# Kernel tuning notes

Measured on AMD Instinct MI355X. Metric: run time of the kernel, lower is better.

## Reference

```python
import jax, jax.numpy as jnp
import numpy as np

N_FEATURE = 1024
N_HEAD = 16
DK = N_FEATURE // N_HEAD
SCALE = float(np.sqrt(DK))
LN_EPS = 1e-5


def setup_inputs() -> dict:
    key = jax.random.key(0)
    ks = jax.random.split(key, 12)
    B, T, F = 4, 2048, N_FEATURE
    s = 1.0 / np.sqrt(F)
    inp = {
        "key": jax.random.normal(ks[0], (B, T, F), jnp.float32),
        "value": jax.random.normal(ks[1], (B, T, F), jnp.float32),
        "query": jax.random.normal(ks[2], (B, T, F), jnp.float32),
        "Wq": jax.random.uniform(ks[3], (F, F), jnp.float32, -s, s),
        "bq": jax.random.uniform(ks[4], (F,), jnp.float32, -s, s),
        "Wk": jax.random.uniform(ks[5], (F, F), jnp.float32, -s, s),
        "bk": jax.random.uniform(ks[6], (F,), jnp.float32, -s, s),
        "Wv": jax.random.uniform(ks[7], (F, F), jnp.float32, -s, s),
        "bv": jax.random.uniform(ks[8], (F,), jnp.float32, -s, s),
        "Wo": jax.random.uniform(ks[9], (F, F), jnp.float32, -s, s),
        "bo": jax.random.uniform(ks[10], (F,), jnp.float32, -s, s),
        "ln_g": jnp.ones((F,), jnp.float32),
        "ln_b": jnp.zeros((F,), jnp.float32),
    }
    return inp


def reference(key, value, query, Wq, bq, Wk, bk, Wv, bv, Wo, bo, ln_g, ln_b):
    # key/value/query: [B, T, F]. torch chunk(n_head, -1) == reshape to (B,T,H,dk).
    B, T, F = query.shape
    residual = query
    q = (query @ Wq.T + bq).reshape(B, T, N_HEAD, DK)
    k = (key @ Wk.T + bk).reshape(B, T, N_HEAD, DK)
    v = (value @ Wv.T + bv).reshape(B, T, N_HEAD, DK)
    # scores: [B, H, Tq, Tk]
    scores = jnp.einsum("bqhd,bkhd->bhqk", q, k) / SCALE
    attn = jax.nn.softmax(scores, axis=-1)
    ctx = jnp.einsum("bhqk,bkhd->bqhd", attn, v).reshape(B, T, F)
    out = ctx @ Wo.T + bo  # dropout in eval mode = identity
    x = residual + out
    mu = jnp.mean(x, axis=-1, keepdims=True)
    var = jnp.mean(jnp.square(x - mu), axis=-1, keepdims=True)
    return (x - mu) * jax.lax.rsqrt(var + LN_EPS) * ln_g + ln_b
```

## Files before the change

kernel.cpp:

```cpp
#include <hip/hip_runtime.h>
#include <hip/hip_bf16.h>
#include <cstdint>
#include <cstddef>

#define DEVI __device__ __forceinline__

typedef __attribute__((ext_vector_type(8))) short short8;
typedef __attribute__((ext_vector_type(4))) float f32x4;
typedef __attribute__((ext_vector_type(16))) float f32x16;
typedef __attribute__((ext_vector_type(4))) unsigned int u32x4;

constexpr int Bz = 4, Tt = 2048, Fd = 1024, Hh = 16, Dk = 64;
constexpr int Mrows = Bz * Tt;
constexpr float QSCALE = 0.18033688011112042f;

DEVI unsigned short f2bf(float f) {
  union { __hip_bfloat16 h; unsigned short u; } cv;
  cv.h = __float2bfloat16(f);
  return cv.u;
}

DEVI unsigned cvtpk(float a, float b) {
  unsigned r;
  asm("v_cvt_pk_bf16_f32 %0, %1, %2" : "=v"(r) : "v"(a), "v"(b));
  return r;
}

DEVI void gl_lds16(const void* g, void* s) {
  __builtin_amdgcn_global_load_lds(
      (const __attribute__((address_space(1))) void*)g,
      (__attribute__((address_space(3))) void*)s, 16, 0, 0);
}

__global__ void cvt4_bf16(const float* __restrict__ s0, unsigned short* __restrict__ d0,
                          const float* __restrict__ s1, unsigned short* __restrict__ d1,
                          const float* __restrict__ s2, unsigned short* __restrict__ d2,
                          const float* __restrict__ s3, unsigned short* __restrict__ d3,
                          int n4) {
  const float* src = blockIdx.y == 0 ? s0 : (blockIdx.y == 1 ? s1 : (blockIdx.y == 2 ? s2 : s3));
  unsigned short* dst = blockIdx.y == 0 ? d0 : (blockIdx.y == 1 ? d1 : (blockIdx.y == 2 ? d2 : d3));
  int i = blockIdx.x * blockDim.x + threadIdx.x;
  int stride = gridDim.x * blockDim.x;
  for (; i < n4; i += stride) {
    float4 v = reinterpret_cast<const float4*>(src)[i];
    ushort4 o;
    o.x = f2bf(v.x); o.y = f2bf(v.y); o.z = f2bf(v.z); o.w = f2bf(v.w);
    reinterpret_cast<ushort4*>(dst)[i] = o;
  }
}

__global__ __launch_bounds__(256, 2) void gemm_qkvf(
    const float* __restrict__ q32, const float* __restrict__ k32,
    const float* __restrict__ v32, const unsigned short* __restrict__ wq,
    const unsigned short* __restrict__ wk, const unsigned short* __restrict__ wv,
    const float* __restrict__ bq, const float* __restrict__ bk, const float* __restrict__ bv,
    unsigned short* __restrict__ Qb, unsigned short* __restrict__ Kb,
    unsigned short* __restrict__ Vt) {
  constexpr int K = 1024, N = 1024;
  __shared__ __align__(16) unsigned short As[128 * 64];
  __shared__ __align__(16) unsigned short Bs[128 * 64];
  int z = blockIdx.z;
  const float* A32 = z == 0 ? q32 : (z == 1 ? k32 : v32);
  const unsigned short* W = z == 0 ? wq : (z == 1 ? wk : wv);
  const float* bias = z == 0 ? bq : (z == 1 ? bk : bv);
  void* out = z == 0 ? (void*)Qb : (z == 1 ? (void*)Kb : (void*)Vt);
  float scale = z == 0 ? QSCALE : 1.0f;
  int mode = z == 2 ? 2 : 0;

  int f = blockIdx.y * gridDim.x + blockIdx.x;
  f = (f & 7) * 64 + (f >> 3);
  const int m0 = (f >> 3) * 128, n0 = (f & 7) * 128;
  const int t = threadIdx.x, w = t >> 6, l = t & 63;
  const int wr = w >> 1, wc = w & 1;
  const int lr = l & 15, lg = l >> 4;
  f32x4 acc[4][4] = {};

  for (int k0 = 0; k0 < K; k0 += 64) {
    __syncthreads();
    float4 fA[4][2];
#pragma unroll
    for (int i = 0; i < 4; ++i) {
      int row = i * 32 + w * 8 + (l >> 3);
      const float* src = A32 + (size_t)(m0 + row) * K + k0 + (l & 7) * 8;
      fA[i][0] = ((const float4*)src)[0];
      fA[i][1] = ((const float4*)src)[1];
    }
#pragma unroll
    for (int i = 0; i < 4; ++i) {
      int base = i * 4096 + w * 1024;
      int d = base + l * 16;
      int row = d >> 7;
      int srcb = ((l & 7) ^ (row & 7)) << 4;
      gl_lds16((const char*)W + ((size_t)(n0 + row) * K + k0) * 2 + srcb, (char*)Bs + base);
    }
#pragma unroll
    for (int i = 0; i < 4; ++i) {
      int row = i * 32 + w * 8 + (l >> 3);
      u32x4 wv4;
      wv4[0] = cvtpk(fA[i][0].x, fA[i][0].y);
      wv4[1] = cvtpk(fA[i][0].z, fA[i][0].w);
      wv4[2] = cvtpk(fA[i][1].x, fA[i][1].y);
      wv4[3] = cvtpk(fA[i][1].z, fA[i][1].w);
      int slot = (l & 7) ^ (row & 7);
      *(u32x4*)((char*)As + row * 128 + slot * 16) = wv4;
    }
    __syncthreads();
#pragma unroll
    for (int kk = 0; kk < 2; ++kk) {
      short8 af[4], bf[4];
#pragma unroll
      for (int i = 0; i < 4; ++i) {
        int ra = wr * 64 + i * 16 + lr;
        int rb = wc * 64 + i * 16 + lr;
        af[i] = *(const short8*)((const char*)As + ra * 128 + (((kk * 4 + lg) ^ (ra & 7)) << 4));
        bf[i] = *(const short8*)((const char*)Bs + rb * 128 + (((kk * 4 + lg) ^ (rb & 7)) << 4));
      }
#pragma unroll
      for (int mi = 0; mi < 4; ++mi)
#pragma unroll
        for (int ni = 0; ni < 4; ++ni)
          acc[mi][ni] = __builtin_amdgcn_mfma_f32_16x16x32_bf16(af[mi], bf[ni], acc[mi][ni], 0, 0, 0);
    }
  }
#pragma unroll
  for (int mi = 0; mi < 4; ++mi)
#pragma unroll
    for (int ni = 0; ni < 4; ++ni) {
      int col = n0 + wc * 64 + ni * 16 + lr;
      float bv = bias[col];
      if (mode == 2) {
        int hh = col >> 6, dd = col & 63;
        int row = m0 + wr * 64 + mi * 16 + lg * 4;
        int bb = row >> 11, t0 = row & 2047;
        ushort4 o;
        o.x = f2bf(acc[mi][ni][0] + bv);
        o.y = f2bf(acc[mi][ni][1] + bv);
        o.z = f2bf(acc[mi][ni][2] + bv);
        o.w = f2bf(acc[mi][ni][3] + bv);
        *(ushort4*)((unsigned short*)out + (((size_t)(bb * Hh + hh) * Dk + dd) << 11) + t0) = o;
      } else {
#pragma unroll
        for (int r = 0; r < 4; ++r) {
          int row = m0 + wr * 64 + mi * 16 + lg * 4 + r;
          ((unsigned short*)out)[(size_t)row * N + col] = f2bf((acc[mi][ni][r] + bv) * scale);
        }
      }
    }
}

__global__ __launch_bounds__(256, 2) void gemm_out(
    const unsigned short* __restrict__ A, const unsigned short* __restrict__ W,
    const float* __restrict__ bias, const float* __restrict__ resid,
    float* __restrict__ out) {
  constexpr int K = 1024, N = 1024;
  __shared__ __align__(16) unsigned short As[128 * 64];
  __shared__ __align__(16) unsigned short Bs[128 * 64];
  int f = blockIdx.y * gridDim.x + blockIdx.x;
  f = (f & 7) * 64 + (f >> 3);
  const int m0 = (f >> 3) * 128, n0 = (f & 7) * 128;
  const int t = threadIdx.x, w = t >> 6, l = t & 63;
  const int wr = w >> 1, wc = w & 1;
  const int lr = l & 15, lg = l >> 4;
  f32x4 acc[4][4] = {};
  for (int k0 = 0; k0 < K; k0 += 64) {
    __syncthreads();
#pragma unroll
    for (int i = 0; i < 4; ++i) {
      int base = i * 4096 + w * 1024;
      int d = base + l * 16;
      int row = d >> 7;
      int srcb = ((l & 7) ^ (row & 7)) << 4;
      gl_lds16((const char*)A + ((size_t)(m0 + row) * K + k0) * 2 + srcb, (char*)As + base);
      gl_lds16((const char*)W + ((size_t)(n0 + row) * K + k0) * 2 + srcb, (char*)Bs + base);
    }
    __syncthreads();
#pragma unroll
    for (int kk = 0; kk < 2; ++kk) {
      short8 af[4], bf[4];
#pragma unroll
      for (int i = 0; i < 4; ++i) {
        int ra = wr * 64 + i * 16 + lr;
        int rb = wc * 64 + i * 16 + lr;
        af[i] = *(const short8*)((const char*)As + ra * 128 + (((kk * 4 + lg) ^ (ra & 7)) << 4));
        bf[i] = *(const short8*)((const char*)Bs + rb * 128 + (((kk * 4 + lg) ^ (rb & 7)) << 4));
      }
#pragma unroll
      for (int mi = 0; mi < 4; ++mi)
#pragma unroll
        for (int ni = 0; ni < 4; ++ni)
          acc[mi][ni] = __builtin_amdgcn_mfma_f32_16x16x32_bf16(af[mi], bf[ni], acc[mi][ni], 0, 0, 0);
    }
  }
#pragma unroll
  for (int mi = 0; mi < 4; ++mi)
#pragma unroll
    for (int ni = 0; ni < 4; ++ni) {
      int col = n0 + wc * 64 + ni * 16 + lr;
      float bv = bias[col];
#pragma unroll
      for (int r = 0; r < 4; ++r) {
        int row = m0 + wr * 64 + mi * 16 + lg * 4 + r;
        size_t idx = (size_t)row * N + col;
        out[idx] = acc[mi][ni][r] + bv + resid[idx];
      }
    }
}

__global__ __launch_bounds__(256, 2) void attn_kernel(
    const unsigned short* __restrict__ Qb, const unsigned short* __restrict__ Kb,
    const unsigned short* __restrict__ Vt, unsigned short* __restrict__ Ctx) {
  __shared__ __align__(16) unsigned short smem[6 * 4096];
  unsigned short* Ks0 = smem;
  unsigned short* Ks1 = smem + 4096;
  unsigned short* Ks2 = smem + 2 * 4096;
  unsigned short* Vs0 = smem + 3 * 4096;
  unsigned short* Vs1 = smem + 4 * 4096;
  unsigned short* Vs2 = smem + 5 * 4096;
  int bid = blockIdx.x;
  bid = (bid & 7) * 64 + (bid >> 3);
  const int q0 = (bid & 7) * 256;
  const int h = (bid >> 3) & 15;
  const int b = bid >> 7;
  const int t = threadIdx.x, w = t >> 6, l = t & 63;
  const int q31 = l & 31, hi = l >> 5;
  const int qbase = q0 + w * 64;

  short8 qfA[4], qfB[4];
  {
    const unsigned short* qpA = Qb + (size_t)(b * Tt + qbase + q31) * Fd + h * Dk;
    const unsigned short* qpB = qpA + (size_t)32 * Fd;
#pragma unroll
    for (int c = 0; c < 4; ++c) {
      qfA[c] = *(const short8*)(qpA + c * 16 + hi * 8);
      qfB[c] = *(const short8*)(qpB + c * 16 + hi * 8);
    }
  }

  int koff[8];
#pragma unroll
  for (int g = 0; g < 2; ++g)
#pragma unroll
    for (int c = 0; c < 4; ++c) {
      int row = g * 32 + q31;
      koff[g * 4 + c] = row * 128 + ((c * 32 + hi * 16) ^ ((row & 7) << 4));
    }

  const size_t kbase = (size_t)(b * Tt) * Fd + h * Dk;
  const size_t vbase = (size_t)((b * Hh + h) * Dk) * Tt;

  f32x16 OA0{}, OA1{}, OB0{}, OB1{};
  float lsA0 = 0.f, lsB0 = 0.f, lsA1 = 0.f, lsB1 = 0.f;

  auto stage = [&](unsigned short* Kd, unsigned short* Vd, int kt) {
#pragma unroll
    for (int i = 0; i < 2; ++i) {
      int base = w * 2048 + i * 1024;
      int d0 = base + l * 16;
      int row = d0 >> 7, inb = d0 & 127;
      int srcb = inb ^ ((row & 7) << 4);
      gl_lds16((const char*)Kb + (kbase + (size_t)(kt * 64 + row) * Fd) * 2 + srcb, (char*)Kd + base);
      gl_lds16((const char*)Vt + (vbase + (size_t)row * Tt + kt * 64) * 2 + srcb, (char*)Vd + base);
    }
  };

  auto softmax_pack = [&](const f32x16& S0, const f32x16& S1, float& lsA, float& lsB, short8* pf) {
    unsigned pk0[8], pk1[8];
#pragma unroll
    for (int j = 0; j < 8; ++j) {
      int r = j * 2;
      float a0 = __builtin_amdgcn_exp2f(S0[r]);
      float a1 = __builtin_amdgcn_exp2f(S0[r + 1]);
      float b0 = __builtin_amdgcn_exp2f(S1[r]);
      float b1 = __builtin_amdgcn_exp2f(S1[r + 1]);
      lsA += a0 + a1;
      lsB += b0 + b1;
      pk0[j] = cvtpk(a0, a1);
      pk1[j] = cvtpk(b0, b1);
    }
#pragma unroll
    for (int kc = 0; kc < 2; ++kc) {
      unsigned a0 = pk0[kc * 4 + 0], a2 = pk0[kc * 4 + 2];
      unsigned a1 = pk0[kc * 4 + 1], a3 = pk0[kc * 4 + 3];
      asm("v_permlane32_swap_b32 %0, %1" : "+v"(a0), "+v"(a2));
      asm("v_permlane32_swap_b32 %0, %1" : "+v"(a1), "+v"(a3));
      unsigned b0 = pk1[kc * 4 + 0], b2 = pk1[kc * 4 + 2];
      unsigned b1 = pk1[kc * 4 + 1], b3 = pk1[kc * 4 + 3];
      asm("v_permlane32_swap_b32 %0, %1" : "+v"(b0), "+v"(b2));
      asm("v_permlane32_swap_b32 %0, %1" : "+v"(b1), "+v"(b3));
      u32x4 fa, fb;
      fa[0] = a0; fa[1] = a1; fa[2] = a2; fa[3] = a3;
      fb[0] = b0; fb[1] = b1; fb[2] = b2; fb[3] = b3;
      pf[kc] = __builtin_bit_cast(short8, fa);
      pf[2 + kc] = __builtin_bit_cast(short8, fb);
    }
  };

  auto tile = [&](const unsigned short* Kd, const unsigned short* Vd) {
    f32x16 S0a{}, S1a{}, S0b{}, S1b{};
    __builtin_amdgcn_s_setprio(1);
#pragma unroll
    for (int c = 0; c < 4; ++c) {
      short8 k0 = *(const short8*)((const char*)Kd + koff[c]);
      short8 k1 = *(const short8*)((const char*)Kd + koff[4 + c]);
      S0a = __builtin_amdgcn_mfma_f32_32x32x16_bf16(k0, qfA[c], S0a, 0, 0, 0);
      S1a = __builtin_amdgcn_mfma_f32_32x32x16_bf16(k1, qfA[c], S1a, 0, 0, 0);
      S0b = __builtin_amdgcn_mfma_f32_32x32x16_bf16(k0, qfB[c], S0b, 0, 0, 0);
      S1b = __builtin_amdgcn_mfma_f32_32x32x16_bf16(k1, qfB[c], S1b, 0, 0, 0);
    }
    __builtin_amdgcn_s_setprio(0);
    short8 pfA[4], pfB[4];
    softmax_pack(S0a, S1a, lsA0, lsB0, pfA);
    softmax_pack(S0b, S1b, lsA1, lsB1, pfB);
    __builtin_amdgcn_s_setprio(1);
#pragma unroll
    for (int db = 0; db < 2; ++db)
#pragma unroll
      for (int kvc = 0; kvc < 4; ++kvc) {
        short8 vf = *(const short8*)((const char*)Vd + koff[db * 4 + kvc]);
        if (db == 0) {
          OA0 = __builtin_amdgcn_mfma_f32_32x32x16_bf16(vf, pfA[kvc], OA0, 0, 0, 0);
          OB0 = __builtin_amdgcn_mfma_f32_32x32x16_bf16(vf, pfB[kvc], OB0, 0, 0, 0);
        } else {
          OA1 = __builtin_amdgcn_mfma_f32_32x32x16_bf16(vf, pfA[kvc], OA1, 0, 0, 0);
          OB1 = __builtin_amdgcn_mfma_f32_32x32x16_bf16(vf, pfB[kvc], OB1, 0, 0, 0);
        }
      }
    __builtin_amdgcn_s_setprio(0);
  };

  stage(Ks0, Vs0, 0);
  stage(Ks1, Vs1, 1);
  unsigned short *kC = Ks0, *vC = Vs0;
  unsigned short *kN = Ks1, *vN = Vs1;
  unsigned short *kW = Ks2, *vW = Vs2;
  for (int kt = 0; kt < 30; ++kt) {
    asm volatile("s_waitcnt vmcnt(4)" ::: "memory");
    __builtin_amdgcn_s_barrier();
    stage(kW, vW, kt + 2);
    tile(kC, vC);
    unsigned short *tk = kC, *tv = vC;
    kC = kN; vC = vN;
    kN = kW; vN = vW;
    kW = tk; vW = tv;
  }
  asm volatile("s_waitcnt vmcnt(4)" ::: "memory");
  __builtin_amdgcn_s_barrier();
  tile(kC, vC);
  asm volatile("s_waitcnt vmcnt(0)" ::: "memory");
  __builtin_amdgcn_s_barrier();
  tile(kN, vN);
  __builtin_amdgcn_s_barrier();

  float ls0 = lsA0 + lsB0;
  ls0 += __shfl_xor(ls0, 32);
  float linv0 = 1.0f / ls0;
  float ls1 = lsA1 + lsB1;
  ls1 += __shfl_xor(ls1, 32);
  float linv1 = 1.0f / ls1;
  unsigned short* Ow = smem + w * 4096;
#pragma unroll
  for (int g = 0; g < 2; ++g) {
    float linv = g == 0 ? linv0 : linv1;
    int rowq = g * 32 + q31;
#pragma unroll
    for (int db = 0; db < 2; ++db)
#pragma unroll
      for (int rp = 0; rp < 8; ++rp) {
        int r = rp * 2;
        float a, b2;
        if (g == 0) {
          a = (db == 0 ? OA0[r] : OA1[r]) * linv;
          b2 = (db == 0 ? OA0[r + 1] : OA1[r + 1]) * linv;
        } else {
          a = (db == 0 ? OB0[r] : OB1[r]) * linv;
          b2 = (db == 0 ? OB0[r + 1] : OB1[r + 1]) * linv;
        }
        unsigned wv = cvtpk(a, b2);
        int dd = db * 32 + (r & 3) + 8 * (r >> 2) + 4 * hi;
        int byteo = (rowq * 128 + (dd >> 1) * 4) ^ ((rowq & 7) << 4);
        *(unsigned*)((char*)Ow + byteo) = wv;
      }
  }
#pragma unroll
  for (int i = 0; i < 8; ++i) {
    int qq = i * 8 + (l >> 3), slot = l & 7;
    int byteo = (qq * 128 + slot * 16) ^ ((qq & 7) << 4);
    short8 ov = *(const short8*)((const char*)Ow + byteo);
    *(short8*)(Ctx + (size_t)(b * Tt + qbase + qq) * Fd + h * Dk + slot * 8) = ov;
  }
}

__global__ __launch_bounds__(256) void ln_res(
    float* __restrict__ xo, const float* __restrict__ gamma, const float* __restrict__ beta) {
  int row = blockIdx.x, t = threadIdx.x;
  float4 xv = ((const float4*)(xo + (size_t)row * Fd))[t];
  float x0 = xv.x, x1 = xv.y, x2 = xv.z, x3 = xv.w;
  float s = x0 + x1 + x2 + x3;
  float ss = x0 * x0 + x1 * x1 + x2 * x2 + x3 * x3;
#pragma unroll
  for (int off = 32; off >= 1; off >>= 1) {
    s += __shfl_xor(s, off);
    ss += __shfl_xor(ss, off);
  }
  __shared__ float rs_[4], rss[4];
  int w = t >> 6, l = t & 63;
  if (l == 0) { rs_[w] = s; rss[w] = ss; }
  __syncthreads();
  s = rs_[0] + rs_[1] + rs_[2] + rs_[3];
  ss = rss[0] + rss[1] + rss[2] + rss[3];
  float mu = s * (1.0f / 1024.0f);
  float var = ss * (1.0f / 1024.0f) - mu * mu;
  float rstd = rsqrtf(var + 1e-5f);
  float4 gv = ((const float4*)gamma)[t];
  float4 bv = ((const float4*)beta)[t];
  float4 o;
  o.x = (x0 - mu) * rstd * gv.x + bv.x;
  o.y = (x1 - mu) * rstd * gv.y + bv.y;
  o.z = (x2 - mu) * rstd * gv.z + bv.z;
  o.w = (x3 - mu) * rstd * gv.w + bv.w;
  ((float4*)(xo + (size_t)row * Fd))[t] = o;
}

extern "C" void kernel_launch(void* const* d_in, const int* in_sizes, int n_in,
                              void* d_out, int out_size, void* d_ws, size_t ws_size,
                              hipStream_t stream) {
  (void)in_sizes; (void)n_in; (void)out_size; (void)ws_size;
  const float* key   = (const float*)d_in[0];
  const float* value = (const float*)d_in[1];
  const float* query = (const float*)d_in[2];
  const float* Wq = (const float*)d_in[3];
  const float* bq = (const float*)d_in[4];
  const float* Wk = (const float*)d_in[5];
  const float* bk = (const float*)d_in[6];
  const float* Wv = (const float*)d_in[7];
  const float* bv_ = (const float*)d_in[8];
  const float* Wo = (const float*)d_in[9];
  const float* bo = (const float*)d_in[10];
  const float* ln_g = (const float*)d_in[11];
  const float* ln_b = (const float*)d_in[12];
  float* out = (float*)d_out;

  char* ws = (char*)d_ws;
  size_t off = 0;
  auto alloc = [&](size_t bytes) {
    char* p = ws + off;
    off += (bytes + 255) & ~(size_t)255;
    return p;
  };
  const size_t MF = (size_t)Mrows * Fd;
  unsigned short* Qb  = (unsigned short*)alloc(MF * 2);
  unsigned short* Kbf = (unsigned short*)alloc(MF * 2);
  unsigned short* Vtb = (unsigned short*)alloc(MF * 2);
  unsigned short* Ctx = (unsigned short*)alloc(MF * 2);
  unsigned short* wqb = (unsigned short*)alloc((size_t)Fd * Fd * 2);
  unsigned short* wkb = (unsigned short*)alloc((size_t)Fd * Fd * 2);
  unsigned short* wvb = (unsigned short*)alloc((size_t)Fd * Fd * 2);
  unsigned short* wob = (unsigned short*)alloc((size_t)Fd * Fd * 2);

  cvt4_bf16<<<dim3(256, 4), 256, 0, stream>>>(Wq, wqb, Wk, wkb, Wv, wvb, Wo, wob, (Fd * Fd) / 4);

  gemm_qkvf<<<dim3(Fd / 128, Mrows / 128, 3), 256, 0, stream>>>(
      query, key, value, wqb, wkb, wvb, bq, bk, bv_, Qb, Kbf, Vtb);

  attn_kernel<<<Bz * Hh * (Tt / 256), 256, 0, stream>>>(Qb, Kbf, Vtb, Ctx);

  gemm_out<<<dim3(Fd / 128, Mrows / 128), 256, 0, stream>>>(Ctx, wob, bo, query, out);
  ln_res<<<Mrows, 256, 0, stream>>>(out, ln_g, ln_b);
}
```

Baseline: 183.1 us.

## Software-pipeline attention loop: overlap QK of next tile with PV of previous

Restructures the attention main loop so each iteration computes QK^T for tile kt, then PV for tile kt-1 using the probabilities packed in the previous iteration, and only then runs softmax on the new scores. This lets the exp/pack VALU work interleave with MFMA work instead of serialising QK→softmax→PV within a tile. To keep tile kt-1's V resident while tile kt+2 is being prefetched, the LDS ring grows from 3 to 4 K/V buffers (64 KB), which may limit occupancy, and pfA/pfB now stay live across iterations, adding register pressure.

```diff
diff --git a/kernel.cpp b/kernel.cpp
--- a/kernel.cpp
+++ b/kernel.cpp
@@ -209,13 +209,7 @@
 __global__ __launch_bounds__(256, 2) void attn_kernel(
     const unsigned short* __restrict__ Qb, const unsigned short* __restrict__ Kb,
     const unsigned short* __restrict__ Vt, unsigned short* __restrict__ Ctx) {
-  __shared__ __align__(16) unsigned short smem[6 * 4096];
-  unsigned short* Ks0 = smem;
-  unsigned short* Ks1 = smem + 4096;
-  unsigned short* Ks2 = smem + 2 * 4096;
-  unsigned short* Vs0 = smem + 3 * 4096;
-  unsigned short* Vs1 = smem + 4 * 4096;
-  unsigned short* Vs2 = smem + 5 * 4096;
+  __shared__ __align__(16) unsigned short smem[8 * 4096];
   int bid = blockIdx.x;
   bid = (bid & 7) * 64 + (bid >> 3);
   const int q0 = (bid & 7) * 256;
@@ -249,18 +243,58 @@
   const size_t vbase = (size_t)((b * Hh + h) * Dk) * Tt;
 
   f32x16 OA0{}, OA1{}, OB0{}, OB1{};
+  short8 pfA[4], pfB[4];
   float lsA0 = 0.f, lsB0 = 0.f, lsA1 = 0.f, lsB1 = 0.f;
 
-  auto stage = [&](unsigned short* Kd, unsigned short* Vd, int kt) {
+  auto kbuf = [&](int kt) { return (const char*)smem + ((kt & 3) << 13); };
+  auto vbuf = [&](int kt) { return (const char*)smem + 32768 + ((kt & 3) << 13); };
+
+  auto stage = [&](int kt) {
+    char* Kd = (char*)smem + ((kt & 3) << 13);
+    char* Vd = (char*)smem + 32768 + ((kt & 3) << 13);
 #pragma unroll
     for (int i = 0; i < 2; ++i) {
       int base = w * 2048 + i * 1024;
       int d0 = base + l * 16;
       int row = d0 >> 7, inb = d0 & 127;
       int srcb = inb ^ ((row & 7) << 4);
-      gl_lds16((const char*)Kb + (kbase + (size_t)(kt * 64 + row) * Fd) * 2 + srcb, (char*)Kd + base);
-      gl_lds16((const char*)Vt + (vbase + (size_t)row * Tt + kt * 64) * 2 + srcb, (char*)Vd + base);
-    }
+      gl_lds16((const char*)Kb + (kbase + (size_t)(kt * 64 + row) * Fd) * 2 + srcb, Kd + base);
+      gl_lds16((const char*)Vt + (vbase + (size_t)row * Tt + kt * 64) * 2 + srcb, Vd + base);
+    }
+  };
+
+  auto qk = [&](int kt, f32x16& S0a, f32x16& S1a, f32x16& S0b, f32x16& S1b) {
+    const char* Kd = kbuf(kt);
+    __builtin_amdgcn_s_setprio(1);
+#pragma unroll
+    for (int c = 0; c < 4; ++c) {
+      short8 k0 = *(const short8*)(Kd + koff[c]);
+      short8 k1 = *(const short8*)(Kd + koff[4 + c]);
+      S0a = __builtin_amdgcn_mfma_f32_32x32x16_bf16(k0, qfA[c], S0a, 0, 0, 0);
+      S1a = __builtin_amdgcn_mfma_f32_32x32x16_bf16(k1, qfA[c], S1a, 0, 0, 0);
+      S0b = __builtin_amdgcn_mfma_f32_32x32x16_bf16(k0, qfB[c], S0b, 0, 0, 0);
+      S1b = __builtin_amdgcn_mfma_f32_32x32x16_bf16(k1, qfB[c], S1b, 0, 0, 0);
+    }
+    __builtin_amdgcn_s_setprio(0);
+  };
+
+  auto pv = [&](int kt) {
+    const char* Vd = vbuf(kt);
+    __builtin_amdgcn_s_setprio(1);
+#pragma unroll
+    for (int db = 0; db < 2; ++db)
+#pragma unroll
+      for (int kvc = 0; kvc < 4; ++kvc) {
+        short8 vf = *(const short8*)(Vd + koff[db * 4 + kvc]);
+        if (db == 0) {
+          OA0 = __builtin_amdgcn_mfma_f32_32x32x16_bf16(vf, pfA[kvc], OA0, 0, 0, 0);
+          OB0 = __builtin_amdgcn_mfma_f32_32x32x16_bf16(vf, pfB[kvc], OB0, 0, 0, 0);
+        } else {
+          OA1 = __builtin_amdgcn_mfma_f32_32x32x16_bf16(vf, pfA[kvc], OA1, 0, 0, 0);
+          OB1 = __builtin_amdgcn_mfma_f32_32x32x16_bf16(vf, pfB[kvc], OB1, 0, 0, 0);
+        }
+      }
+    __builtin_amdgcn_s_setprio(0);
   };
 
   auto softmax_pack = [&](const f32x16& S0, const f32x16& S1, float& lsA, float& lsB, short8* pf) {
@@ -295,60 +329,37 @@
     }
   };
 
-  auto tile = [&](const unsigned short* Kd, const unsigned short* Vd) {
+  stage(0);
+  stage(1);
+  asm volatile("s_waitcnt vmcnt(4)" ::: "memory");
+  __builtin_amdgcn_s_barrier();
+  stage(2);
+  {
     f32x16 S0a{}, S1a{}, S0b{}, S1b{};
-    __builtin_amdgcn_s_setprio(1);
-#pragma unroll
-    for (int c = 0; c < 4; ++c) {
-      short8 k0 = *(const short8*)((const char*)Kd + koff[c]);
-      short8 k1 = *(const short8*)((const char*)Kd + koff[4 + c]);
-      S0a = __builtin_amdgcn_mfma_f32_32x32x16_bf16(k0, qfA[c], S0a, 0, 0, 0);
-      S1a = __builtin_amdgcn_mfma_f32_32x32x16_bf16(k1, qfA[c], S1a, 0, 0, 0);
-      S0b = __builtin_amdgcn_mfma_f32_32x32x16_bf16(k0, qfB[c], S0b, 0, 0, 0);
-      S1b = __builtin_amdgcn_mfma_f32_32x32x16_bf16(k1, qfB[c], S1b, 0, 0, 0);
-    }
-    __builtin_amdgcn_s_setprio(0);
-    short8 pfA[4], pfB[4];
+    qk(0, S0a, S1a, S0b, S1b);
     softmax_pack(S0a, S1a, lsA0, lsB0, pfA);
     softmax_pack(S0b, S1b, lsA1, lsB1, pfB);
-    __builtin_amdgcn_s_setprio(1);
-#pragma unroll
-    for (int db = 0; db < 2; ++db)
-#pragma unroll
-      for (int kvc = 0; kvc < 4; ++kvc) {
-        short8 vf = *(const short8*)((const char*)Vd + koff[db * 4 + kvc]);
-        if (db == 0) {
-          OA0 = __builtin_amdgcn_mfma_f32_32x32x16_bf16(vf, pfA[kvc], OA0, 0, 0, 0);
-          OB0 = __builtin_amdgcn_mfma_f32_32x32x16_bf16(vf, pfB[kvc], OB0, 0, 0, 0);
-        } else {
-          OA1 = __builtin_amdgcn_mfma_f32_32x32x16_bf16(vf, pfA[kvc], OA1, 0, 0, 0);
-          OB1 = __builtin_amdgcn_mfma_f32_32x32x16_bf16(vf, pfB[kvc], OB1, 0, 0, 0);
-        }
-      }
-    __builtin_amdgcn_s_setprio(0);
-  };
-
-  stage(Ks0, Vs0, 0);
-  stage(Ks1, Vs1, 1);
-  unsigned short *kC = Ks0, *vC = Vs0;
-  unsigned short *kN = Ks1, *vN = Vs1;
-  unsigned short *kW = Ks2, *vW = Vs2;
-  for (int kt = 0; kt < 30; ++kt) {
+  }
+  for (int kt = 1; kt < 31; ++kt) {
     asm volatile("s_waitcnt vmcnt(4)" ::: "memory");
     __builtin_amdgcn_s_barrier();
-    stage(kW, vW, kt + 2);
-    tile(kC, vC);
-    unsigned short *tk = kC, *tv = vC;
-    kC = kN; vC = vN;
-    kN = kW; vN = vW;
-    kW = tk; vW = tv;
-  }
-  asm volatile("s_waitcnt vmcnt(4)" ::: "memory");
-  __builtin_amdgcn_s_barrier();
-  tile(kC, vC);
+    if (kt < 30) stage(kt + 2);
+    f32x16 S0a{}, S1a{}, S0b{}, S1b{};
+    qk(kt, S0a, S1a, S0b, S1b);
+    pv(kt - 1);
+    softmax_pack(S0a, S1a, lsA0, lsB0, pfA);
+    softmax_pack(S0b, S1b, lsA1, lsB1, pfB);
+  }
   asm volatile("s_waitcnt vmcnt(0)" ::: "memory");
   __builtin_amdgcn_s_barrier();
-  tile(kN, vN);
+  {
+    f32x16 S0a{}, S1a{}, S0b{}, S1b{};
+    qk(31, S0a, S1a, S0b, S1b);
+    pv(30);
+    softmax_pack(S0a, S1a, lsA0, lsB0, pfA);
+    softmax_pack(S0b, S1b, lsA1, lsB1, pfB);
+  }
+  pv(31);
   __builtin_amdgcn_s_barrier();
 
   float ls0 = lsA0 + lsB0;
```

New measurement: 183.0 us. About the same (-0.1%).
